# Optimization experiments

Measured on AMD Instinct MI355X. Metric: run time of the kernel, lower is better.

The kernel has to match this reference:

```python
import jax, jax.numpy as jnp
import numpy as np

IN_DIM = 1024
K = 8
QK_DIM = IN_DIM // K  # 128


def setup_inputs() -> dict:
    key = jax.random.key(0)
    ks = jax.random.split(key, 8)
    B, C, L = 8, IN_DIM, 2048
    d = QK_DIM
    s_in = 1.0 / np.sqrt(C)  # torch Conv1d default init scale (kaiming-uniform-ish)
    x = jax.random.normal(ks[0], (B, C, L), dtype=jnp.float32)
    Wq = jax.random.uniform(ks[1], (d, C), jnp.float32, -s_in, s_in)
    bq = jax.random.uniform(ks[2], (d,), jnp.float32, -s_in, s_in)
    Wk = jax.random.uniform(ks[3], (d, C), jnp.float32, -s_in, s_in)
    bk = jax.random.uniform(ks[4], (d,), jnp.float32, -s_in, s_in)
    Wv = jax.random.uniform(ks[5], (C, C), jnp.float32, -s_in, s_in)
    bv = jax.random.uniform(ks[6], (C,), jnp.float32, -s_in, s_in)
    gamma = jnp.zeros((1,), dtype=jnp.float32)  # nn.Parameter(torch.zeros(1))
    return {"x": x, "Wq": Wq, "bq": bq, "Wk": Wk, "bk": bk, "Wv": Wv, "bv": bv, "gamma": gamma}


def reference(x, Wq, bq, Wk, bk, Wv, bv, gamma):
    # x: [B, C, L]; 1x1 Conv1d == per-position linear over channels
    q = jnp.einsum("dc,bcl->bld", Wq, x) + bq  # proj_query permuted: [B, L, d]
    k = jnp.einsum("dc,bcl->bdl", Wk, x) + bk[None, :, None]  # [B, d, L]
    v = jnp.einsum("oc,bcl->bol", Wv, x) + bv[None, :, None]  # [B, C, L]
    energy = jnp.einsum("bld,bdm->blm", q, k)  # unscaled attention logits [B, L, L]
    attention = jax.nn.softmax(energy, axis=-1)  # softmax over keys
    # out = bmm(V, attention^T): out[b,c,j] = sum_l attention[b,j,l] * v[b,c,l]
    out = jnp.einsum("bcl,bjl->bcj", v, attention)  # [B, C, L]
    return gamma * out + x
```

## Files before the change

kernel.cpp:

```cpp
#include <hip/hip_runtime.h>
#include <hip/hip_bf16.h>
#include <stdint.h>

#define B_SZ 8
#define C_SZ 1024
#define L_SZ 2048
#define D_SZ 128
#define LOG2E 1.44269504088896f

typedef const float* __restrict__ fpp;
typedef __hip_bfloat16 bf16;
typedef short s8v __attribute__((ext_vector_type(8)));
typedef float f4v __attribute__((ext_vector_type(4)));

#define MFMA __builtin_amdgcn_mfma_f32_16x16x32_bf16

#define GLOAD16(gp, lp) __builtin_amdgcn_global_load_lds(                  \
    (const __attribute__((address_space(1))) void*)(gp),                   \
    (__attribute__((address_space(3))) void*)(lp), 16, 0, 0)

__global__ __launch_bounds__(256) void prep_kernel(
    fpp Wq, fpp Wk, fpp Wv, fpp bq, fpp bk, fpp bv,
    bf16* __restrict__ Wcat, float* __restrict__ bcat) {
  const int bidx = blockIdx.x;
  if (bidx < 1280) {
    fpp src; float scale = 1.0f;
    if (bidx < 128)      { src = Wq + (size_t)bidx * C_SZ; scale = LOG2E; }
    else if (bidx < 256) { src = Wk + (size_t)(bidx - 128) * C_SZ; }
    else                 { src = Wv + (size_t)(bidx - 256) * C_SZ; }
    const float4 v = reinterpret_cast<const float4*>(src)[threadIdx.x];
    bf16 o[4] = {__float2bfloat16(v.x * scale), __float2bfloat16(v.y * scale),
                 __float2bfloat16(v.z * scale), __float2bfloat16(v.w * scale)};
    reinterpret_cast<uint2*>(Wcat + (size_t)bidx * C_SZ)[threadIdx.x] =
        *reinterpret_cast<uint2*>(o);
  } else {
    const int i = (bidx - 1280) * 256 + threadIdx.x;
    if (i < 128)        bcat[i] = bq[i] * LOG2E;
    else if (i < 256)   bcat[i] = bk[i - 128];
    else if (i < 1280)  bcat[i] = bv[i - 256];
  }
}

__global__ __launch_bounds__(256) void transpose_kernel(fpp x, bf16* __restrict__ xT) {
  const int b  = blockIdx.z;
  const int l0 = blockIdx.x * 32;
  const int c0 = blockIdx.y * 32;
  __shared__ float T[32][33];
  const int t = threadIdx.x;
  const int r  = t >> 3;
  const int cg = (t & 7) * 4;
  const float4 v = *reinterpret_cast<const float4*>(
      x + ((size_t)b * C_SZ + c0 + r) * L_SZ + l0 + cg);
  T[r][cg + 0] = v.x; T[r][cg + 1] = v.y; T[r][cg + 2] = v.z; T[r][cg + 3] = v.w;
  __syncthreads();
  bf16 o[4];
#pragma unroll
  for (int i = 0; i < 4; ++i) o[i] = __float2bfloat16(T[cg + i][r]);
  *reinterpret_cast<uint2*>(
      xT + ((size_t)b * L_SZ + l0 + r) * C_SZ + c0 + cg) = *reinterpret_cast<uint2*>(o);
}

__global__ __launch_bounds__(256) void proj_kernel(
    const bf16* __restrict__ xTb, const bf16* __restrict__ Wcat, fpp bcat,
    bf16* __restrict__ Qt, bf16* __restrict__ Kt, bf16* __restrict__ Vt) {
  __shared__ bf16 Als[128 * 64];
  __shared__ bf16 Bls[128 * 64];
  const int bid = blockIdx.x;
  const int tid = threadIdx.x, wid = tid >> 6, lane = tid & 63;
  const int lm = lane & 15, lg = lane >> 4;
  const int wm = wid >> 1, wn = wid & 1;
  const bool isQK = bid < 256;

  const bf16 *Arow, *Brow;
  int m0, n0;
  if (isQK) {
    m0 = (bid & 1) * 128;
    n0 = (bid >> 1) * 128;
    Arow = Wcat; Brow = xTb;
  } else {
    const int v = bid - 256;
    m0 = (v >> 3) * 128;
    n0 = (v & 7) * 128;
    Arow = xTb; Brow = Wcat + (size_t)256 * C_SZ;
  }

  const int srow = lane >> 3;
  const int scol = (lane & 7) * 8;

  f4v acc[4][4] = {};
  for (int k0 = 0; k0 < C_SZ; k0 += 64) {
    __syncthreads();
#pragma unroll
    for (int ch = 0; ch < 4; ++ch) {
      const int chunk = wid * 4 + ch;
      const int row = chunk * 8 + srow;
      GLOAD16(Arow + (size_t)(m0 + row) * C_SZ + k0 + scol, &Als[chunk * 512]);
      GLOAD16(Brow + (size_t)(n0 + row) * C_SZ + k0 + scol, &Bls[chunk * 512]);
    }
    __syncthreads();
#pragma unroll
    for (int kc = 0; kc < 2; ++kc) {
      s8v af[4], bfr[4];
#pragma unroll
      for (int i = 0; i < 4; ++i) {
        af[i]  = *reinterpret_cast<const s8v*>(
            &Als[(wm * 64 + i * 16 + lm) * 64 + kc * 32 + lg * 8]);
        bfr[i] = *reinterpret_cast<const s8v*>(
            &Bls[(wn * 64 + i * 16 + lm) * 64 + kc * 32 + lg * 8]);
      }
#pragma unroll
      for (int a = 0; a < 4; ++a)
#pragma unroll
        for (int bj = 0; bj < 4; ++bj)
          acc[a][bj] = MFMA(af[a], bfr[bj], acc[a][bj], 0, 0, 0);
    }
  }

  if (isQK) {
    bf16* dst = (m0 == 0) ? Qt : Kt;
#pragma unroll
    for (int a = 0; a < 4; ++a) {
      const int d = m0 + wm * 64 + a * 16 + lg * 4;
      const int dd = d & 127;
      const float4 bb = *reinterpret_cast<const float4*>(bcat + d);
#pragma unroll
      for (int bj = 0; bj < 4; ++bj) {
        const int gl = n0 + wn * 64 + bj * 16 + lm;
        bf16 o[4] = {__float2bfloat16(acc[a][bj][0] + bb.x),
                     __float2bfloat16(acc[a][bj][1] + bb.y),
                     __float2bfloat16(acc[a][bj][2] + bb.z),
                     __float2bfloat16(acc[a][bj][3] + bb.w)};
        *reinterpret_cast<uint2*>(dst + (size_t)gl * D_SZ + dd) =
            *reinterpret_cast<uint2*>(o);
      }
    }
  } else {
#pragma unroll
    for (int a = 0; a < 4; ++a) {
      const int gl = m0 + wm * 64 + a * 16 + lg * 4;
      const int b = gl >> 11, l = gl & 2047;
#pragma unroll
      for (int bj = 0; bj < 4; ++bj) {
        const int c = n0 + wn * 64 + bj * 16 + lm;
        const float bvc = bcat[256 + c];
        bf16 o[4] = {__float2bfloat16(acc[a][bj][0] + bvc),
                     __float2bfloat16(acc[a][bj][1] + bvc),
                     __float2bfloat16(acc[a][bj][2] + bvc),
                     __float2bfloat16(acc[a][bj][3] + bvc)};
        *reinterpret_cast<uint2*>(Vt + ((size_t)b * C_SZ + c) * L_SZ + l) =
            *reinterpret_cast<uint2*>(o);
      }
    }
  }
}

__global__ __launch_bounds__(256) void pv_kernel(
    const bf16* __restrict__ Qt, const bf16* __restrict__ Kt,
    const bf16* __restrict__ Vt,
    fpp x, fpp gamma, float* __restrict__ out) {
  const int gid = blockIdx.x;
  const int b  = gid & 7;
  const int ct = (gid >> 3) & 3;
  const int qt = gid >> 5;
  const int j0 = qt * 64;
  const int c0 = ct * 256;
  const int tid = threadIdx.x, wid = tid >> 6, lane = tid & 63;
  const int lm = lane & 15, lg = lane >> 4;

  __shared__ bf16 Plds[2][64][64];
  __shared__ bf16 Qlds[64][128];
  __shared__ float lred[4][4][16];
  __shared__ float linv_lds[64];
  char* const Pbase = (char*)&Plds[0][0][0];
  char* const Qbase = (char*)&Qlds[0][0];

  const int swz = (lm & 7) << 4;
  const int wr_off = (wid * 32 + lg * 8) ^ swz;

  {
    const int r  = tid >> 2;
    const int cb = (tid & 3) * 64;
    const bf16* src = Qt + ((size_t)b * L_SZ + j0 + r) * D_SZ + cb / 2;
#pragma unroll
    for (int j = 0; j < 4; ++j) {
      const s8v w = *reinterpret_cast<const s8v*>(src + j * 8);
      const int co = cb + j * 16;
      *reinterpret_cast<s8v*>(Qbase + r * 256 + (co ^ ((r & 15) << 4))) = w;
    }
  }

  f4v acc[4][4] = {};
  float lsum[4] = {0.f, 0.f, 0.f, 0.f};
  s8v kbA[4], kbB[4];
  const bf16* Vbase = Vt + ((size_t)b * C_SZ + c0 + wid * 64) * L_SZ;
  const bf16* Kbase = Kt + (size_t)b * L_SZ * D_SZ;

#pragma unroll
  for (int dc = 0; dc < 4; ++dc)
    kbA[dc] = *reinterpret_cast<const s8v*>(
        Kbase + (size_t)(wid * 16 + lm) * D_SZ + dc * 32 + lg * 8);
  __syncthreads();

#define PV_ITER(nn, KCUR, KNXT)                                                \
  {                                                                            \
    const int n = (nn);                                                        \
    const int k0 = n * 64;                                                     \
    const int slot = (nn) & 1;                                                 \
                               \
    s8v vfrag[2][4];                                                           \
    _Pragma("unroll") for (int kc = 0; kc < 2; ++kc)                           \
      _Pragma("unroll") for (int nt = 0; nt < 4; ++nt)                         \
        vfrag[kc][nt] = *reinterpret_cast<const s8v*>(                         \
            Vbase + (size_t)(nt * 16 + lm) * L_SZ + k0 + kc * 32 + lg * 8);    \
                                    \
    if (n + 1 < 32) {                                                          \
      _Pragma("unroll") for (int dc = 0; dc < 4; ++dc)                         \
        KNXT[dc] = *reinterpret_cast<const s8v*>(                              \
            Kbase + (size_t)(k0 + 64 + wid * 16 + lm) * D_SZ + dc * 32 + lg * 8); \
    }                                                                          \
                                \
    f4v s[4] = {};                                                             \
    _Pragma("unroll") for (int dc = 0; dc < 4; ++dc) {                         \
      _Pragma("unroll") for (int nq = 0; nq < 4; ++nq) {                       \
        const int row = nq * 16 + lm;                                          \
        const s8v bQf = *reinterpret_cast<const s8v*>(                         \
            Qbase + row * 256 + ((dc * 64 + lg * 16) ^ ((row & 15) << 4)));    \
        s[nq] = MFMA(KCUR[dc], bQf, s[nq], 0, 0, 0);                           \
      }                                                                        \
    }                                                                          \
                       \
    _Pragma("unroll") for (int nq = 0; nq < 4; ++nq) {                         \
      float p0 = __builtin_amdgcn_exp2f(s[nq][0]);                             \
      float p1 = __builtin_amdgcn_exp2f(s[nq][1]);                             \
      float p2 = __builtin_amdgcn_exp2f(s[nq][2]);                             \
      float p3 = __builtin_amdgcn_exp2f(s[nq][3]);                             \
      lsum[nq] += (p0 + p1) + (p2 + p3);                                       \
      uint2 pw;                                                                \
      pw.x = ((__float_as_uint(p0) + 0x8000u) >> 16) |                         \
             ((__float_as_uint(p1) + 0x8000u) & 0xFFFF0000u);                  \
      pw.y = ((__float_as_uint(p2) + 0x8000u) >> 16) |                         \
             ((__float_as_uint(p3) + 0x8000u) & 0xFFFF0000u);                  \
      *reinterpret_cast<uint2*>(                                               \
          Pbase + slot * 8192 + (nq * 16 + lm) * 128 + wr_off) = pw;           \
    }                                                                          \
    __syncthreads();                                                           \
                        \
    __builtin_amdgcn_s_setprio(1);                                             \
    _Pragma("unroll") for (int kc = 0; kc < 2; ++kc) {                         \
      const int rd_off = (kc * 64 + lg * 16) ^ swz;                            \
      s8v aP[4];                                                               \
      _Pragma("unroll") for (int mq = 0; mq < 4; ++mq)                         \
        aP[mq] = *reinterpret_cast<const s8v*>(                                \
            Pbase + slot * 8192 + (mq * 16 + lm) * 128 + rd_off);              \
      _Pragma("unroll") for (int nt = 0; nt < 4; ++nt)                         \
        _Pragma("unroll") for (int mq = 0; mq < 4; ++mq)                       \
          acc[mq][nt] = MFMA(aP[mq], vfrag[kc][nt], acc[mq][nt], 0, 0, 0);     \
    }                                                                          \
    __builtin_amdgcn_s_setprio(0);                                             \
  }

  for (int it = 0; it < 16; ++it) {
    PV_ITER(2 * it,     kbA, kbB);
    PV_ITER(2 * it + 1, kbB, kbA);
  }
#undef PV_ITER

#pragma unroll
  for (int nq = 0; nq < 4; ++nq) {
    lsum[nq] += __shfl_xor(lsum[nq], 16);
    lsum[nq] += __shfl_xor(lsum[nq], 32);
  }
  if (lg == 0) {
#pragma unroll
    for (int nq = 0; nq < 4; ++nq) lred[wid][nq][lm] = lsum[nq];
  }
  __syncthreads();
  if (tid < 64) {
    const int nq = tid >> 4, l2 = tid & 15;
    linv_lds[tid] = 1.0f /
        (lred[0][nq][l2] + lred[1][nq][l2] + lred[2][nq][l2] + lred[3][nq][l2]);
  }
  __syncthreads();

  const float g = gamma[0];
#pragma unroll
  for (int mq = 0; mq < 4; ++mq) {
    float li[4];
#pragma unroll
    for (int r = 0; r < 4; ++r) li[r] = linv_lds[mq * 16 + lg * 4 + r];
#pragma unroll
    for (int nt = 0; nt < 4; ++nt) {
      const int c = c0 + wid * 64 + nt * 16 + lm;
      const int j = j0 + mq * 16 + lg * 4;
      const size_t off = ((size_t)b * C_SZ + c) * L_SZ + j;
      const float4 xv = *reinterpret_cast<const float4*>(x + off);
      float4 o;
      o.x = g * (acc[mq][nt][0] * li[0]) + xv.x;
      o.y = g * (acc[mq][nt][1] * li[1]) + xv.y;
      o.z = g * (acc[mq][nt][2] * li[2]) + xv.z;
      o.w = g * (acc[mq][nt][3] * li[3]) + xv.w;
      *reinterpret_cast<float4*>(out + off) = o;
    }
  }
}

extern "C" void kernel_launch(void* const* d_in, const int* in_sizes, int n_in,
                              void* d_out, int out_size, void* d_ws,
                              size_t ws_size, hipStream_t stream) {
  fpp x     = (fpp)d_in[0];
  fpp Wq    = (fpp)d_in[1];
  fpp bq    = (fpp)d_in[2];
  fpp Wk    = (fpp)d_in[3];
  fpp bk    = (fpp)d_in[4];
  fpp Wv    = (fpp)d_in[5];
  fpp bv    = (fpp)d_in[6];
  fpp gamma = (fpp)d_in[7];
  float* out = (float*)d_out;

  bf16* xTb  = (bf16*)d_out;
  bf16* Wcat = xTb + (size_t)B_SZ * L_SZ * C_SZ;
  bf16* Qt = (bf16*)d_ws;
  bf16* Kt = Qt + (size_t)B_SZ * L_SZ * D_SZ;
  bf16* Vt = Kt + (size_t)B_SZ * L_SZ * D_SZ;
  float* bcat = (float*)(Vt + (size_t)B_SZ * C_SZ * L_SZ);

  const dim3 blk(256);
  prep_kernel<<<dim3(1285), blk, 0, stream>>>(Wq, Wk, Wv, bq, bk, bv, Wcat, bcat);
  transpose_kernel<<<dim3(L_SZ / 32, C_SZ / 32, B_SZ), blk, 0, stream>>>(x, xTb);
  proj_kernel<<<dim3(256 + 1024), blk, 0, stream>>>(xTb, Wcat, bcat, Qt, Kt, Vt);
  pv_kernel<<<dim3(B_SZ * 4 * (L_SZ / 64)), blk, 0, stream>>>(
      Qt, Kt, Vt, x, gamma, out);
}
```

Before: 299.2 us.

## Compute attention once per query tile across all channels with 512-thread blocks

Each pv_kernel block now uses 8 waves covering all 1024 channels for a 64-query tile, instead of four channel-split blocks that each recomputed the QK^T scores and exp. Key chunks grow to 128 per iteration, and V fragments are double-buffered in registers per 32-wide sub-chunk to overlap global loads with MFMAs. This removes the 4x redundant score and softmax computation, but it doubles accumulator registers per thread (launch bounds 512,2) and cuts the grid to 256 blocks, which may hurt occupancy and latency hiding.

```diff
diff --git a/kernel.cpp b/kernel.cpp
--- a/kernel.cpp
+++ b/kernel.cpp
@@ -154,116 +154,115 @@
   }
 }
 
-__global__ __launch_bounds__(256) void pv_kernel(
+__global__ __launch_bounds__(512, 2) void pv_kernel(
     const bf16* __restrict__ Qt, const bf16* __restrict__ Kt,
     const bf16* __restrict__ Vt,
     fpp x, fpp gamma, float* __restrict__ out) {
   const int gid = blockIdx.x;
   const int b  = gid & 7;
-  const int ct = (gid >> 3) & 3;
-  const int qt = gid >> 5;
+  const int qt = gid >> 3;
   const int j0 = qt * 64;
-  const int c0 = ct * 256;
   const int tid = threadIdx.x, wid = tid >> 6, lane = tid & 63;
   const int lm = lane & 15, lg = lane >> 4;
 
-  __shared__ bf16 Plds[2][64][64];
   __shared__ bf16 Qlds[64][128];
-  __shared__ float lred[4][4][16];
+  __shared__ bf16 Plds[2][64][128];
+  __shared__ float lred[8][4][16];
   __shared__ float linv_lds[64];
+  char* const Qbase = (char*)&Qlds[0][0];
   char* const Pbase = (char*)&Plds[0][0][0];
-  char* const Qbase = (char*)&Qlds[0][0];
 
   const int swz = (lm & 7) << 4;
-  const int wr_off = (wid * 32 + lg * 8) ^ swz;
 
   {
-    const int r  = tid >> 2;
-    const int cb = (tid & 3) * 64;
+    const int r  = tid >> 3;
+    const int cb = (tid & 7) * 32;
     const bf16* src = Qt + ((size_t)b * L_SZ + j0 + r) * D_SZ + cb / 2;
-#pragma unroll
-    for (int j = 0; j < 4; ++j) {
-      const s8v w = *reinterpret_cast<const s8v*>(src + j * 8);
-      const int co = cb + j * 16;
-      *reinterpret_cast<s8v*>(Qbase + r * 256 + (co ^ ((r & 15) << 4))) = w;
-    }
-  }
-
-  f4v acc[4][4] = {};
+    const int m = (r & 7) << 4;
+    *reinterpret_cast<s8v*>(Qbase + r * 256 + (cb ^ m)) =
+        *reinterpret_cast<const s8v*>(src);
+    *reinterpret_cast<s8v*>(Qbase + r * 256 + ((cb + 16) ^ m)) =
+        *reinterpret_cast<const s8v*>(src + 8);
+  }
+
+  f4v acc[4][8] = {};
   float lsum[4] = {0.f, 0.f, 0.f, 0.f};
-  s8v kbA[4], kbB[4];
-  const bf16* Vbase = Vt + ((size_t)b * C_SZ + c0 + wid * 64) * L_SZ;
+  s8v kreg[4];
+  s8v va[8], vb[8];
   const bf16* Kbase = Kt + (size_t)b * L_SZ * D_SZ;
+  const bf16* Vbase = Vt + ((size_t)b * C_SZ + wid * 128) * L_SZ;
 
 #pragma unroll
   for (int dc = 0; dc < 4; ++dc)
-    kbA[dc] = *reinterpret_cast<const s8v*>(
+    kreg[dc] = *reinterpret_cast<const s8v*>(
         Kbase + (size_t)(wid * 16 + lm) * D_SZ + dc * 32 + lg * 8);
   __syncthreads();
 
-#define PV_ITER(nn, KCUR, KNXT)                                                \
-  {                                                                            \
-    const int n = (nn);                                                        \
-    const int k0 = n * 64;                                                     \
-    const int slot = (nn) & 1;                                                 \
-                               \
-    s8v vfrag[2][4];                                                           \
-    _Pragma("unroll") for (int kc = 0; kc < 2; ++kc)                           \
-      _Pragma("unroll") for (int nt = 0; nt < 4; ++nt)                         \
-        vfrag[kc][nt] = *reinterpret_cast<const s8v*>(                         \
-            Vbase + (size_t)(nt * 16 + lm) * L_SZ + k0 + kc * 32 + lg * 8);    \
-                                    \
-    if (n + 1 < 32) {                                                          \
-      _Pragma("unroll") for (int dc = 0; dc < 4; ++dc)                         \
-        KNXT[dc] = *reinterpret_cast<const s8v*>(                              \
-            Kbase + (size_t)(k0 + 64 + wid * 16 + lm) * D_SZ + dc * 32 + lg * 8); \
-    }                                                                          \
-                                \
-    f4v s[4] = {};                                                             \
-    _Pragma("unroll") for (int dc = 0; dc < 4; ++dc) {                         \
-      _Pragma("unroll") for (int nq = 0; nq < 4; ++nq) {                       \
-        const int row = nq * 16 + lm;                                          \
-        const s8v bQf = *reinterpret_cast<const s8v*>(                         \
-            Qbase + row * 256 + ((dc * 64 + lg * 16) ^ ((row & 15) << 4)));    \
-        s[nq] = MFMA(KCUR[dc], bQf, s[nq], 0, 0, 0);                           \
-      }                                                                        \
-    }                                                                          \
-                       \
-    _Pragma("unroll") for (int nq = 0; nq < 4; ++nq) {                         \
-      float p0 = __builtin_amdgcn_exp2f(s[nq][0]);                             \
-      float p1 = __builtin_amdgcn_exp2f(s[nq][1]);                             \
-      float p2 = __builtin_amdgcn_exp2f(s[nq][2]);                             \
-      float p3 = __builtin_amdgcn_exp2f(s[nq][3]);                             \
-      lsum[nq] += (p0 + p1) + (p2 + p3);                                       \
-      uint2 pw;                                                                \
-      pw.x = ((__float_as_uint(p0) + 0x8000u) >> 16) |                         \
-             ((__float_as_uint(p1) + 0x8000u) & 0xFFFF0000u);                  \
-      pw.y = ((__float_as_uint(p2) + 0x8000u) >> 16) |                         \
-             ((__float_as_uint(p3) + 0x8000u) & 0xFFFF0000u);                  \
-      *reinterpret_cast<uint2*>(                                               \
-          Pbase + slot * 8192 + (nq * 16 + lm) * 128 + wr_off) = pw;           \
-    }                                                                          \
-    __syncthreads();                                                           \
-                        \
-    __builtin_amdgcn_s_setprio(1);                                             \
-    _Pragma("unroll") for (int kc = 0; kc < 2; ++kc) {                         \
-      const int rd_off = (kc * 64 + lg * 16) ^ swz;                            \
+#define LOADV(BUF, K0, KC)                                                     \
+  _Pragma("unroll") for (int nt = 0; nt < 8; ++nt)                             \
+    BUF[nt] = *reinterpret_cast<const s8v*>(                                   \
+        Vbase + (size_t)(nt * 16 + lm) * L_SZ + (K0) + (KC)*32 + lg * 8);
+
+  for (int n = 0; n < 16; ++n) {
+    const int k0 = n * 128;
+    char* const Pslot = Pbase + (n & 1) * 16384;
+
+    LOADV(va, k0, 0);
+
+    f4v s[4] = {};
+#pragma unroll
+    for (int dc = 0; dc < 4; ++dc) {
+#pragma unroll
+      for (int nq = 0; nq < 4; ++nq) {
+        const int row = nq * 16 + lm;
+        const s8v bQf = *reinterpret_cast<const s8v*>(
+            Qbase + row * 256 + ((dc * 64 + lg * 16) ^ ((row & 7) << 4)));
+        s[nq] = MFMA(kreg[dc], bQf, s[nq], 0, 0, 0);
+      }
+    }
+    if (n + 1 < 16) {
+#pragma unroll
+      for (int dc = 0; dc < 4; ++dc)
+        kreg[dc] = *reinterpret_cast<const s8v*>(
+            Kbase + (size_t)(k0 + 128 + wid * 16 + lm) * D_SZ + dc * 32 + lg * 8);
+    }
+#pragma unroll
+    for (int nq = 0; nq < 4; ++nq) {
+      float p0 = __builtin_amdgcn_exp2f(s[nq][0]);
+      float p1 = __builtin_amdgcn_exp2f(s[nq][1]);
+      float p2 = __builtin_amdgcn_exp2f(s[nq][2]);
+      float p3 = __builtin_amdgcn_exp2f(s[nq][3]);
+      lsum[nq] += (p0 + p1) + (p2 + p3);
+      uint2 pw;
+      pw.x = ((__float_as_uint(p0) + 0x8000u) >> 16) |
+             ((__float_as_uint(p1) + 0x8000u) & 0xFFFF0000u);
+      pw.y = ((__float_as_uint(p2) + 0x8000u) >> 16) |
+             ((__float_as_uint(p3) + 0x8000u) & 0xFFFF0000u);
+      *reinterpret_cast<uint2*>(
+          Pslot + (nq * 16 + lm) * 256 + ((wid * 32 + lg * 8) ^ swz)) = pw;
+    }
+    __syncthreads();
+
+    __builtin_amdgcn_s_setprio(1);
+#define PV_KC(KC, CUR, NXT, LAST)                                              \
+    {                                                                          \
+      if (!(LAST)) { LOADV(NXT, k0, (KC) + 1); }                               \
       s8v aP[4];                                                               \
       _Pragma("unroll") for (int mq = 0; mq < 4; ++mq)                         \
         aP[mq] = *reinterpret_cast<const s8v*>(                                \
-            Pbase + slot * 8192 + (mq * 16 + lm) * 128 + rd_off);              \
-      _Pragma("unroll") for (int nt = 0; nt < 4; ++nt)                         \
+            Pslot + (mq * 16 + lm) * 256 + (((KC)*64 + lg * 16) ^ swz));       \
+      _Pragma("unroll") for (int nt = 0; nt < 8; ++nt)                         \
         _Pragma("unroll") for (int mq = 0; mq < 4; ++mq)                       \
-          acc[mq][nt] = MFMA(aP[mq], vfrag[kc][nt], acc[mq][nt], 0, 0, 0);     \
-    }                                                                          \
-    __builtin_amdgcn_s_setprio(0);                                             \
-  }
-
-  for (int it = 0; it < 16; ++it) {
-    PV_ITER(2 * it,     kbA, kbB);
-    PV_ITER(2 * it + 1, kbB, kbA);
-  }
-#undef PV_ITER
+          acc[mq][nt] = MFMA(aP[mq], CUR[nt], acc[mq][nt], 0, 0, 0);           \
+    }
+    PV_KC(0, va, vb, false);
+    PV_KC(1, vb, va, false);
+    PV_KC(2, va, vb, false);
+    PV_KC(3, vb, va, true);
+#undef PV_KC
+    __builtin_amdgcn_s_setprio(0);
+  }
+#undef LOADV
 
 #pragma unroll
   for (int nq = 0; nq < 4; ++nq) {
@@ -277,8 +276,10 @@
   __syncthreads();
   if (tid < 64) {
     const int nq = tid >> 4, l2 = tid & 15;
-    linv_lds[tid] = 1.0f /
-        (lred[0][nq][l2] + lred[1][nq][l2] + lred[2][nq][l2] + lred[3][nq][l2]);
+    float s = 0.f;
+#pragma unroll
+    for (int w = 0; w < 8; ++w) s += lred[w][nq][l2];
+    linv_lds[tid] = 1.0f / s;
   }
   __syncthreads();
 
@@ -289,8 +290,8 @@
 #pragma unroll
     for (int r = 0; r < 4; ++r) li[r] = linv_lds[mq * 16 + lg * 4 + r];
 #pragma unroll
-    for (int nt = 0; nt < 4; ++nt) {
-      const int c = c0 + wid * 64 + nt * 16 + lm;
+    for (int nt = 0; nt < 8; ++nt) {
+      const int c = wid * 128 + nt * 16 + lm;
       const int j = j0 + mq * 16 + lg * 4;
       const size_t off = ((size_t)b * C_SZ + c) * L_SZ + j;
       const float4 xv = *reinterpret_cast<const float4*>(x + off);
@@ -328,6 +329,6 @@
   prep_kernel<<<dim3(1285), blk, 0, stream>>>(Wq, Wk, Wv, bq, bk, bv, Wcat, bcat);
   transpose_kernel<<<dim3(L_SZ / 32, C_SZ / 32, B_SZ), blk, 0, stream>>>(x, xTb);
   proj_kernel<<<dim3(256 + 1024), blk, 0, stream>>>(xTb, Wcat, bcat, Qt, Kt, Vt);
-  pv_kernel<<<dim3(B_SZ * 4 * (L_SZ / 64)), blk, 0, stream>>>(
+  pv_kernel<<<dim3(B_SZ * (L_SZ / 64)), dim3(512), 0, stream>>>(
       Qt, Kt, Vt, x, gamma, out);
 }
```

Result: faster. 263.9 us (median of 3 runs) (-11.8%).
